# Performance work log

Hardware: AMD Instinct MI355X
Metric: run time of the kernel (lower is better)

Reference implementation:

```python
import jax, jax.numpy as jnp
import numpy as np

D_MODEL = 1024
NUM_HEADS = 16
D_HEAD = D_MODEL // NUM_HEADS


def setup_inputs() -> dict:
    key = jax.random.key(0)
    ks = jax.random.split(key, 5)
    s = 1.0 / np.sqrt(D_MODEL)
    x = jax.random.normal(ks[0], (4, 2048, D_MODEL), dtype=jnp.float32)
    w_qkv = jax.random.uniform(ks[1], (D_MODEL, 3 * D_MODEL), jnp.float32, -s, s)
    b_qkv = jax.random.uniform(ks[2], (3 * D_MODEL,), jnp.float32, -s, s)
    w_out = jax.random.uniform(ks[3], (D_MODEL, D_MODEL), jnp.float32, -s, s)
    b_out = jax.random.uniform(ks[4], (D_MODEL,), jnp.float32, -s, s)
    return {"x": x, "w_qkv": w_qkv, "b_qkv": b_qkv, "w_out": w_out, "b_out": b_out}


def reference(x, w_qkv, b_qkv, w_out, b_out):
    B, L, D = x.shape
    qkv = x @ w_qkv + b_qkv  # [B, L, 3D]
    qkv = qkv.reshape(B, L, 3, NUM_HEADS, D_HEAD)
    q, k, v = qkv[:, :, 0], qkv[:, :, 1], qkv[:, :, 2]  # [B, L, H, Dh]
    scores = jnp.einsum("bqhd,bkhd->bhqk", q, k) / np.sqrt(D_HEAD).astype(np.float32)
    attn = jax.nn.softmax(scores, axis=-1)
    out = jnp.einsum("bhqk,bkhd->bqhd", attn, v).reshape(B, L, D)
    return out @ w_out + b_out
```

## Files before the change

kernel.cpp:

```cpp
#include <hip/hip_runtime.h>
#include <stdint.h>

typedef unsigned short u16;
typedef __attribute__((ext_vector_type(8))) short bh8;
typedef __attribute__((ext_vector_type(4))) float f4;

#define LOG2E 1.44269504088896f
#define QSCALE 0.18033688f

__device__ inline u16 f2bf(float f) {
  union { float f; uint32_t u; } c; c.f = f;
  uint32_t u = c.u;
  return (u16)((u + 0x7fffu + ((u >> 16) & 1u)) >> 16);
}

__device__ inline float fast_exp2(float x) {
#if __has_builtin(__builtin_amdgcn_exp2f)
  return __builtin_amdgcn_exp2f(x);
#else
  return exp2f(x);
#endif
}

#if __has_builtin(__builtin_amdgcn_global_load_lds)
#define GLD16(gp, lp) __builtin_amdgcn_global_load_lds( \
    (const __attribute__((address_space(1))) void*)(gp), \
    (__attribute__((address_space(3))) void*)(lp), 16, 0, 0)
#else
#define GLD16(gp, lp) do { *(bh8*)(lp) = *(const bh8*)(gp); } while (0)
#endif


__global__ __launch_bounds__(256) void cvt_f32_bf16(const float* __restrict__ src,
                                                    u16* __restrict__ dst, int n4) {
  int i = blockIdx.x * 256 + threadIdx.x;
  if (i < n4) {
    float4 v = ((const float4*)src)[i];
    ushort4 o;
    o.x = f2bf(v.x); o.y = f2bf(v.y); o.z = f2bf(v.z); o.w = f2bf(v.w);
    ((ushort4*)dst)[i] = o;
  }
}

__global__ __launch_bounds__(1024) void transpose_cvt(const float* __restrict__ src,
                                                      u16* __restrict__ dst, int K, int N) {
  __shared__ float tile[32][33];
  int n0 = blockIdx.x * 32, k0 = blockIdx.y * 32;
  int tx = threadIdx.x, ty = threadIdx.y;
  tile[ty][tx] = src[(size_t)(k0 + ty) * N + n0 + tx];
  __syncthreads();
  dst[(size_t)(n0 + ty) * K + k0 + tx] = f2bf(tile[tx][ty]);
}

__global__ __launch_bounds__(1024) void transpose_b16(const u16* __restrict__ src,
                                                      u16* __restrict__ dst) {
  __shared__ u16 t[32][33];
  int bh = blockIdx.z, l0 = blockIdx.y * 32, d0 = blockIdx.x * 32;
  int tx = threadIdx.x, ty = threadIdx.y;
  t[ty][tx] = src[((size_t)bh * 2048 + l0 + ty) * 64 + d0 + tx];
  __syncthreads();
  dst[((size_t)bh * 64 + d0 + ty) * 2048 + l0 + tx] = t[tx][ty];
}

__device__ inline void gemm_mainloop(const u16* __restrict__ A, const u16* __restrict__ Bt,
                                     int K, int m0, int n0,
                                     u16* As, u16* Bs, f4 acc[4][4]) {
  const int tid  = threadIdx.x;
  const int lane = tid & 63;
  const int quad = lane >> 4;
  const int ml   = lane & 15;
  const int wave = tid >> 6;
  const int wm   = (wave >> 1) * 64;
  const int wn   = (wave & 1) * 64;

#pragma unroll 1
  for (int k0 = 0; k0 < K; k0 += 64) {
#pragma unroll
    for (int r = 0; r < 4; ++r) {
      int chunk = r * 256 + tid;
      int row = chunk >> 3, cc = chunk & 7;
      int cg = cc ^ (row & 7);
      GLD16(A + (size_t)(m0 + row) * K + k0 + cg * 8, As + chunk * 8);
    }
#pragma unroll
    for (int r = 0; r < 4; ++r) {
      int chunk = r * 256 + tid;
      int row = chunk >> 3, cc = chunk & 7;
      int cg = cc ^ (row & 7);
      GLD16(Bt + (size_t)(n0 + row) * K + k0 + cg * 8, Bs + chunk * 8);
    }
    __syncthreads();
#pragma unroll
    for (int ks = 0; ks < 2; ++ks) {
      bh8 af[4], bfr[4];
      int cs = (ks * 4 + quad) ^ (ml & 7);
#pragma unroll
      for (int i = 0; i < 4; ++i) {
        int row = wm + i * 16 + ml;
        af[i] = *(const bh8*)(As + (row * 8 + cs) * 8);
      }
#pragma unroll
      for (int j = 0; j < 4; ++j) {
        int row = wn + j * 16 + ml;
        bfr[j] = *(const bh8*)(Bs + (row * 8 + cs) * 8);
      }
#pragma unroll
      for (int i = 0; i < 4; ++i)
#pragma unroll
        for (int j = 0; j < 4; ++j)
          acc[i][j] = __builtin_amdgcn_mfma_f32_16x16x32_bf16(af[i], bfr[j], acc[i][j], 0, 0, 0);
    }
    __syncthreads();
  }
}

__global__ __launch_bounds__(256) void gemm_qkv(const u16* __restrict__ xb,
                                                const u16* __restrict__ wqt,
                                                const float* __restrict__ bqkv,
                                                u16* __restrict__ q, u16* __restrict__ k,
                                                u16* __restrict__ v) {
  __shared__ __align__(16) u16 smem[2 * 128 * 64];
  const f4 fzero = {0.f, 0.f, 0.f, 0.f};
  f4 acc[4][4];
#pragma unroll
  for (int i = 0; i < 4; ++i)
#pragma unroll
    for (int j = 0; j < 4; ++j) acc[i][j] = fzero;

  int m0 = blockIdx.y * 128, n0 = blockIdx.x * 128;
  gemm_mainloop(xb, wqt, 1024, m0, n0, smem, smem + 128 * 64, acc);

  const int lane = threadIdx.x & 63, wave = threadIdx.x >> 6;
  const int quad = lane >> 4, ml = lane & 15;
  const int wm = (wave >> 1) * 64, wn = (wave & 1) * 64;
  u16* dst = (n0 < 1024) ? q : ((n0 < 2048) ? k : v);
  float scale = (n0 < 1024) ? QSCALE : 1.0f;
#pragma unroll
  for (int j = 0; j < 4; ++j) {
    int nn = n0 + wn + j * 16 + ml;
    int h = (nn >> 6) & 15, d = nn & 63;
    float bias = bqkv[nn];
#pragma unroll
    for (int i = 0; i < 4; ++i) {
#pragma unroll
      for (int r = 0; r < 4; ++r) {
        int tok = m0 + wm + i * 16 + quad * 4 + r;
        int b = tok >> 11, l = tok & 2047;
        int bh = b * 16 + h;
        dst[((size_t)bh * 2048 + l) * 64 + d] = f2bf((acc[i][j][r] + bias) * scale);
      }
    }
  }
}

__global__ __launch_bounds__(256) void gemm_out(const u16* __restrict__ ob,
                                                const u16* __restrict__ wot,
                                                const float* __restrict__ bout,
                                                float* __restrict__ out) {
  __shared__ __align__(16) u16 smem[2 * 128 * 64];
  const f4 fzero = {0.f, 0.f, 0.f, 0.f};
  f4 acc[4][4];
#pragma unroll
  for (int i = 0; i < 4; ++i)
#pragma unroll
    for (int j = 0; j < 4; ++j) acc[i][j] = fzero;

  int m0 = blockIdx.y * 128, n0 = blockIdx.x * 128;
  gemm_mainloop(ob, wot, 1024, m0, n0, smem, smem + 128 * 64, acc);

  const int lane = threadIdx.x & 63, wave = threadIdx.x >> 6;
  const int quad = lane >> 4, ml = lane & 15;
  const int wm = (wave >> 1) * 64, wn = (wave & 1) * 64;
#pragma unroll
  for (int j = 0; j < 4; ++j) {
    int nn = n0 + wn + j * 16 + ml;
    float bias = bout[nn];
#pragma unroll
    for (int i = 0; i < 4; ++i)
#pragma unroll
      for (int r = 0; r < 4; ++r) {
        int tok = m0 + wm + i * 16 + quad * 4 + r;
        out[(size_t)tok * 1024 + nn] = acc[i][j][r] + bias;
      }
  }
}

__global__ __launch_bounds__(256) void attn(const u16* __restrict__ q,
                                            const u16* __restrict__ k,
                                            const u16* __restrict__ vt,
                                            u16* __restrict__ o) {
  __shared__ __align__(16) u16 Ks[2][64 * 64];
  __shared__ __align__(16) u16 Vs[2][64 * 64];
  __shared__ __align__(16) u16 Pq[4][16 * 64];
  const int bh = blockIdx.x;
  const int b = bh >> 4, h = bh & 15;
  const int tid = threadIdx.x;
  const int wave = tid >> 6, lane = tid & 63;
  const int quad = lane >> 4, ml = lane & 15;
  const int qw = blockIdx.y * 64 + wave * 16;
  const u16* qp = q + (size_t)bh * 2048 * 64;
  const u16* kp = k + (size_t)bh * 2048 * 64;
  const u16* vp = vt + (size_t)bh * 64 * 2048;
  const f4 fzero = {0.f, 0.f, 0.f, 0.f};

  bh8 qf[2];
#pragma unroll
  for (int ks = 0; ks < 2; ++ks)
    qf[ks] = *(const bh8*)&qp[(size_t)(qw + ml) * 64 + ks * 32 + quad * 8];

  f4 oaccT[4];
#pragma unroll
  for (int j = 0; j < 4; ++j) oaccT[j] = fzero;
  float lsum = 0.f;

  const int srow = tid >> 3, scc = tid & 7;
  const int scg = scc ^ (srow & 7);
  u16* pq = &Pq[wave][ml * 64];
  const int mlsw = ml & 14;

#pragma unroll
  for (int r = 0; r < 2; ++r) {
    int row = r * 32 + srow;
    GLD16(kp + (size_t)row * 64 + scg * 8, &Ks[0][(row * 8 + scc) * 8]);
    GLD16(vp + (size_t)row * 2048 + scg * 8, &Vs[0][(row * 8 + scc) * 8]);
  }
  __syncthreads();

  int cur = 0;
#pragma unroll 1
  for (int t = 0; t < 32; ++t) {
    if (t < 31) {
      int ktn = (t + 1) * 64;
#pragma unroll
      for (int r = 0; r < 2; ++r) {
        int row = r * 32 + srow;
        GLD16(kp + (size_t)(ktn + row) * 64 + scg * 8, &Ks[cur ^ 1][(row * 8 + scc) * 8]);
        GLD16(vp + (size_t)row * 2048 + ktn + scg * 8, &Vs[cur ^ 1][(row * 8 + scc) * 8]);
      }
    }

    f4 s[4];
#pragma unroll
    for (int j = 0; j < 4; ++j) s[j] = fzero;
#pragma unroll
    for (int ks = 0; ks < 2; ++ks) {
      int cs = (ks * 4 + quad) ^ (ml & 7);
      bh8 kf[4];
#pragma unroll
      for (int j = 0; j < 4; ++j)
        kf[j] = *(const bh8*)(&Ks[cur][((j * 16 + ml) * 8 + cs) * 8]);
#pragma unroll
      for (int j = 0; j < 4; ++j)
        s[j] = __builtin_amdgcn_mfma_f32_16x16x32_bf16(kf[j], qf[ks], s[j], 0, 0, 0);
    }

#pragma unroll
    for (int j = 0; j < 4; ++j) {
      uint32_t w[4];
#pragma unroll
      for (int r = 0; r < 4; ++r) {
        float p = fast_exp2(s[j][r]);
        union { float f; uint32_t u; } c; c.f = p;
        c.u = (c.u + 0x8000u) & 0xFFFF0000u;
        lsum += c.f;
        w[r] = c.u;
      }
      int slot = (4 * j + quad) ^ mlsw;
      uint2 pk;
      pk.x = (w[0] >> 16) | (w[1] & 0xFFFF0000u);
      pk.y = (w[2] >> 16) | (w[3] & 0xFFFF0000u);
      *(uint2*)(pq + slot * 4) = pk;
    }

#pragma unroll
    for (int ks = 0; ks < 2; ++ks) {
      int cs = (ks * 4 + quad) ^ (ml & 7);
      bh8 vf[4];
#pragma unroll
      for (int j = 0; j < 4; ++j)
        vf[j] = *(const bh8*)(&Vs[cur][((j * 16 + ml) * 8 + cs) * 8]);
      int ps = (8 * ks + 2 * quad) ^ mlsw;
      bh8 pf = *(const bh8*)(pq + ps * 4);
#pragma unroll
      for (int j = 0; j < 4; ++j)
        oaccT[j] = __builtin_amdgcn_mfma_f32_16x16x32_bf16(vf[j], pf, oaccT[j], 0, 0, 0);
    }
    __syncthreads();
    cur ^= 1;
  }

  lsum += __shfl_xor(lsum, 16, 64);
  lsum += __shfl_xor(lsum, 32, 64);
  float inv = 1.0f / lsum;

  size_t obase = (((size_t)b * 2048 + qw + ml) * 16 + h) * 64;
#pragma unroll
  for (int j = 0; j < 4; ++j) {
    ushort4 w;
    w.x = f2bf(oaccT[j][0] * inv);
    w.y = f2bf(oaccT[j][1] * inv);
    w.z = f2bf(oaccT[j][2] * inv);
    w.w = f2bf(oaccT[j][3] * inv);
    *(ushort4*)(o + obase + j * 16 + quad * 4) = w;
  }
}


extern "C" void kernel_launch(void* const* d_in, const int* in_sizes, int n_in,
                              void* d_out, int out_size, void* d_ws, size_t ws_size,
                              hipStream_t stream) {
  const float* x     = (const float*)d_in[0];
  const float* w_qkv = (const float*)d_in[1];
  const float* b_qkv = (const float*)d_in[2];
  const float* w_out = (const float*)d_in[3];
  const float* b_out = (const float*)d_in[4];
  float* out = (float*)d_out;

  u16* ws  = (u16*)d_ws;
  u16* xb  = ws;
  u16* wqt = xb + (size_t)8192 * 1024;
  u16* wot = wqt + (size_t)3072 * 1024;
  u16* qb  = wot + (size_t)1024 * 1024;
  u16* kb  = qb + (size_t)64 * 2048 * 64;
  u16* vb  = kb + (size_t)64 * 2048 * 64;
  u16* vtb = xb;
  u16* ob  = vb;

  cvt_f32_bf16<<<8192, 256, 0, stream>>>(x, xb, 8192 * 1024 / 4);
  transpose_cvt<<<dim3(96, 32), dim3(32, 32), 0, stream>>>(w_qkv, wqt, 1024, 3072);
  transpose_cvt<<<dim3(32, 32), dim3(32, 32), 0, stream>>>(w_out, wot, 1024, 1024);
  gemm_qkv<<<dim3(24, 64), 256, 0, stream>>>(xb, wqt, b_qkv, qb, kb, vb);
  transpose_b16<<<dim3(2, 64, 64), dim3(32, 32), 0, stream>>>(vb, vtb);
  attn<<<dim3(64, 32), 256, 0, stream>>>(qb, kb, vtb, ob);
  gemm_out<<<dim3(8, 64), 256, 0, stream>>>(ob, wot, b_out, out);
}
```

Before: 313.8 us.

## Process two query groups per wave and load V directly from global

```diff
diff --git a/kernel.cpp b/kernel.cpp
--- a/kernel.cpp
+++ b/kernel.cpp
@@ -185,123 +185,152 @@
   }
 }
 
-__global__ __launch_bounds__(256) void attn(const u16* __restrict__ q,
-                                            const u16* __restrict__ k,
-                                            const u16* __restrict__ vt,
-                                            u16* __restrict__ o) {
+__global__ __launch_bounds__(256, 4) void attn(const u16* __restrict__ q,
+                                               const u16* __restrict__ k,
+                                               const u16* __restrict__ vt,
+                                               u16* __restrict__ o) {
   __shared__ __align__(16) u16 Ks[2][64 * 64];
-  __shared__ __align__(16) u16 Vs[2][64 * 64];
-  __shared__ __align__(16) u16 Pq[4][16 * 64];
+  __shared__ __align__(16) u16 Pq[4][32 * 64];
   const int bh = blockIdx.x;
   const int b = bh >> 4, h = bh & 15;
   const int tid = threadIdx.x;
   const int wave = tid >> 6, lane = tid & 63;
   const int quad = lane >> 4, ml = lane & 15;
-  const int qw = blockIdx.y * 64 + wave * 16;
+  const int qw = blockIdx.y * 128 + wave * 32;
   const u16* qp = q + (size_t)bh * 2048 * 64;
   const u16* kp = k + (size_t)bh * 2048 * 64;
   const u16* vp = vt + (size_t)bh * 64 * 2048;
   const f4 fzero = {0.f, 0.f, 0.f, 0.f};
 
-  bh8 qf[2];
-#pragma unroll
-  for (int ks = 0; ks < 2; ++ks)
-    qf[ks] = *(const bh8*)&qp[(size_t)(qw + ml) * 64 + ks * 32 + quad * 8];
-
-  f4 oaccT[4];
-#pragma unroll
-  for (int j = 0; j < 4; ++j) oaccT[j] = fzero;
-  float lsum = 0.f;
+  const int mlx = ml & 7;
+  const bool mlh = (ml & 8) != 0;
+  const int hb = (((quad & 1) ^ (mlh ? 1 : 0)) << 2);
+  const int qv = quad >> 1;
+
+  bh8 qf[2][2];
+#pragma unroll
+  for (int g = 0; g < 2; ++g)
+#pragma unroll
+    for (int ks = 0; ks < 2; ++ks)
+      qf[g][ks] = *(const bh8*)&qp[(size_t)(qw + g * 16 + ml) * 64 + ks * 32 + quad * 8];
+
+  f4 oacc[2][4];
+#pragma unroll
+  for (int g = 0; g < 2; ++g)
+#pragma unroll
+    for (int j = 0; j < 4; ++j) oacc[g][j] = fzero;
+  float lsum[2] = {0.f, 0.f};
 
   const int srow = tid >> 3, scc = tid & 7;
   const int scg = scc ^ (srow & 7);
   u16* pq = &Pq[wave][ml * 64];
-  const int mlsw = ml & 14;
 
 #pragma unroll
   for (int r = 0; r < 2; ++r) {
     int row = r * 32 + srow;
     GLD16(kp + (size_t)row * 64 + scg * 8, &Ks[0][(row * 8 + scc) * 8]);
-    GLD16(vp + (size_t)row * 2048 + scg * 8, &Vs[0][(row * 8 + scc) * 8]);
   }
   __syncthreads();
 
   int cur = 0;
 #pragma unroll 1
   for (int t = 0; t < 32; ++t) {
+    const int kt = t * 64;
     if (t < 31) {
-      int ktn = (t + 1) * 64;
+      int ktn = kt + 64;
 #pragma unroll
       for (int r = 0; r < 2; ++r) {
         int row = r * 32 + srow;
         GLD16(kp + (size_t)(ktn + row) * 64 + scg * 8, &Ks[cur ^ 1][(row * 8 + scc) * 8]);
-        GLD16(vp + (size_t)row * 2048 + ktn + scg * 8, &Vs[cur ^ 1][(row * 8 + scc) * 8]);
-      }
-    }
-
-    f4 s[4];
-#pragma unroll
-    for (int j = 0; j < 4; ++j) s[j] = fzero;
+      }
+    }
+
+    f4 s[2][4];
+#pragma unroll
+    for (int g = 0; g < 2; ++g)
+#pragma unroll
+      for (int j = 0; j < 4; ++j) s[g][j] = fzero;
 #pragma unroll
     for (int ks = 0; ks < 2; ++ks) {
-      int cs = (ks * 4 + quad) ^ (ml & 7);
+      int cs = (ks * 4 + quad) ^ mlx;
       bh8 kf[4];
 #pragma unroll
       for (int j = 0; j < 4; ++j)
         kf[j] = *(const bh8*)(&Ks[cur][((j * 16 + ml) * 8 + cs) * 8]);
 #pragma unroll
-      for (int j = 0; j < 4; ++j)
-        s[j] = __builtin_amdgcn_mfma_f32_16x16x32_bf16(kf[j], qf[ks], s[j], 0, 0, 0);
-    }
-
-#pragma unroll
-    for (int j = 0; j < 4; ++j) {
-      uint32_t w[4];
-#pragma unroll
-      for (int r = 0; r < 4; ++r) {
-        float p = fast_exp2(s[j][r]);
-        union { float f; uint32_t u; } c; c.f = p;
-        c.u = (c.u + 0x8000u) & 0xFFFF0000u;
-        lsum += c.f;
-        w[r] = c.u;
-      }
-      int slot = (4 * j + quad) ^ mlsw;
-      uint2 pk;
-      pk.x = (w[0] >> 16) | (w[1] & 0xFFFF0000u);
-      pk.y = (w[2] >> 16) | (w[3] & 0xFFFF0000u);
-      *(uint2*)(pq + slot * 4) = pk;
+      for (int j = 0; j < 4; ++j) {
+        s[0][j] = __builtin_amdgcn_mfma_f32_16x16x32_bf16(kf[j], qf[0][ks], s[0][j], 0, 0, 0);
+        s[1][j] = __builtin_amdgcn_mfma_f32_16x16x32_bf16(kf[j], qf[1][ks], s[1][j], 0, 0, 0);
+      }
+    }
+
+    bh8 vf0[4];
+#pragma unroll
+    for (int j = 0; j < 4; ++j)
+      vf0[j] = *(const bh8*)&vp[(size_t)(j * 16 + ml) * 2048 + kt + quad * 8];
+
+    bh8 vf1[4];
+#pragma unroll
+    for (int g = 0; g < 2; ++g) {
+#pragma unroll
+      for (int j = 0; j < 4; ++j) {
+        uint32_t w[4];
+#pragma unroll
+        for (int r = 0; r < 4; ++r) {
+          float p = fast_exp2(s[g][j][r]);
+          union { float f; uint32_t u; } c; c.f = p;
+          c.u = (c.u + 0x8000u) & 0xFFFF0000u;
+          lsum[g] += c.f;
+          w[r] = c.u;
+        }
+        uint2 pk;
+        pk.x = (w[0] >> 16) | (w[1] & 0xFFFF0000u);
+        pk.y = (w[2] >> 16) | (w[3] & 0xFFFF0000u);
+        *(uint2*)(pq + g * 1024 + (((2 * j + qv) ^ mlx) << 3) + hb) = pk;
+      }
+      if (g == 0) {
+#pragma unroll
+        for (int j = 0; j < 4; ++j)
+          vf1[j] = *(const bh8*)&vp[(size_t)(j * 16 + ml) * 2048 + kt + 32 + quad * 8];
+      }
     }
 
 #pragma unroll
     for (int ks = 0; ks < 2; ++ks) {
-      int cs = (ks * 4 + quad) ^ (ml & 7);
-      bh8 vf[4];
-#pragma unroll
-      for (int j = 0; j < 4; ++j)
-        vf[j] = *(const bh8*)(&Vs[cur][((j * 16 + ml) * 8 + cs) * 8]);
-      int ps = (8 * ks + 2 * quad) ^ mlsw;
-      bh8 pf = *(const bh8*)(pq + ps * 4);
-#pragma unroll
-      for (int j = 0; j < 4; ++j)
-        oaccT[j] = __builtin_amdgcn_mfma_f32_16x16x32_bf16(vf[j], pf, oaccT[j], 0, 0, 0);
+#pragma unroll
+      for (int g = 0; g < 2; ++g) {
+        union { uint4 u; bh8 v; } pf;
+        uint4 tp = *(const uint4*)(pq + g * 1024 + (((4 * ks + quad) ^ mlx) << 3));
+        pf.u.x = mlh ? tp.z : tp.x;
+        pf.u.y = mlh ? tp.w : tp.y;
+        pf.u.z = mlh ? tp.x : tp.z;
+        pf.u.w = mlh ? tp.y : tp.w;
+#pragma unroll
+        for (int j = 0; j < 4; ++j) {
+          const bh8 vfj = ks ? vf1[j] : vf0[j];
+          oacc[g][j] = __builtin_amdgcn_mfma_f32_16x16x32_bf16(vfj, pf.v, oacc[g][j], 0, 0, 0);
+        }
+      }
     }
     __syncthreads();
     cur ^= 1;
   }
 
-  lsum += __shfl_xor(lsum, 16, 64);
-  lsum += __shfl_xor(lsum, 32, 64);
-  float inv = 1.0f / lsum;
-
-  size_t obase = (((size_t)b * 2048 + qw + ml) * 16 + h) * 64;
-#pragma unroll
-  for (int j = 0; j < 4; ++j) {
-    ushort4 w;
-    w.x = f2bf(oaccT[j][0] * inv);
-    w.y = f2bf(oaccT[j][1] * inv);
-    w.z = f2bf(oaccT[j][2] * inv);
-    w.w = f2bf(oaccT[j][3] * inv);
-    *(ushort4*)(o + obase + j * 16 + quad * 4) = w;
+#pragma unroll
+  for (int g = 0; g < 2; ++g) {
+    lsum[g] += __shfl_xor(lsum[g], 16, 64);
+    lsum[g] += __shfl_xor(lsum[g], 32, 64);
+    float inv = 1.0f / lsum[g];
+    size_t obase = (((size_t)b * 2048 + qw + g * 16 + ml) * 16 + h) * 64;
+#pragma unroll
+    for (int j = 0; j < 4; ++j) {
+      ushort4 w;
+      w.x = f2bf(oacc[g][j][0] * inv);
+      w.y = f2bf(oacc[g][j][1] * inv);
+      w.z = f2bf(oacc[g][j][2] * inv);
+      w.w = f2bf(oacc[g][j][3] * inv);
+      *(ushort4*)(o + obase + j * 16 + quad * 4) = w;
+    }
   }
 }
 
@@ -331,6 +360,6 @@
   transpose_cvt<<<dim3(32, 32), dim3(32, 32), 0, stream>>>(w_out, wot, 1024, 1024);
   gemm_qkv<<<dim3(24, 64), 256, 0, stream>>>(xb, wqt, b_qkv, qb, kb, vb);
   transpose_b16<<<dim3(2, 64, 64), dim3(32, 32), 0, stream>>>(vb, vtb);
-  attn<<<dim3(64, 32), 256, 0, stream>>>(qb, kb, vtb, ob);
+  attn<<<dim3(64, 16), 256, 0, stream>>>(qb, kb, vtb, ob);
   gemm_out<<<dim3(8, 64), 256, 0, stream>>>(ob, wot, b_out, out);
 }
```

New measurement: 349.5 us. 1.11x slower.
